# Optimization experiments

Measured on AMD Instinct MI355X. Metric: run time of the kernel, lower is better.

Reference implementation:

```python
import jax, jax.numpy as jnp
from jax import lax
import numpy as np

B, H, W, C = 32, 384, 384, 8
FIELD = 7
NUM_ITERS = 5


def setup_inputs() -> dict:
    key = jax.random.key(0)
    k1, k2, k3 = jax.random.split(key, 3)
    x = jax.random.normal(k1, (B, H, W, C), dtype=jnp.float32)
    # k_internal: [field, field, C_in, C_out]; original init is zeros, use small
    # random values so the mean-field iterations are non-trivial.
    k_internal = jax.random.normal(k2, (FIELD, FIELD, C, C), dtype=jnp.float32) * 0.02
    # 1x1 conv (k_scale) weight + bias
    k_scale_w = jax.random.normal(k3, (C, C), dtype=jnp.float32) * (1.0 / np.sqrt(C))
    k_scale_b = jnp.zeros((C,), dtype=jnp.float32)
    return {"x": x, "k_internal": k_internal, "k_scale_w": k_scale_w,
            "k_scale_b": k_scale_b, "num_iters": NUM_ITERS}


def reference(x, k_internal, k_scale_w, k_scale_b, num_iters):
    C_ = x.shape[-1]
    # off-diagonal channel-pair mask, broadcast over spatial kernel dims
    mask = (1.0 - jnp.eye(C_, dtype=x.dtype))[None, None]  # [1,1,C,C]
    k = k_internal * mask
    q = jax.nn.softmax(x, axis=-1)                 # [B,H,W,C]
    u = -jnp.log(jnp.clip(q, 1e-6, 1.0))           # unary potentials
    logits = x
    for _ in range(num_iters):
        penalty = lax.conv_general_dilated(
            q, k, window_strides=(1, 1), padding='SAME',
            dimension_numbers=('NHWC', 'HWIO', 'NHWC'))
        logits = -(u + penalty)
        logits = jnp.einsum('bhwc,cd->bhwd', logits, k_scale_w) + k_scale_b
        q = jax.nn.softmax(logits, axis=-1)
    return logits
```

## Files before the change

kernel.cpp:

```cpp
#include <hip/hip_runtime.h>
#include <math.h>

#define Cc     8
#define FIELD  7
#define PAD    3
#define TW     32
#define TH     16
#define HAW    38
#define HAH    22
#define QSTR   39
#define NSTG   (HAH*QSTR)
#define BB     32
#define HH     384
#define WW     384
#define NB     4
#define NSLOT  64
#define UCLIP  13.815510557964274f

typedef __attribute__((ext_vector_type(8))) short short8;
typedef __attribute__((ext_vector_type(4))) float f32x4;

__device__ __forceinline__ unsigned short f2bf(float f) {
    unsigned u = __float_as_uint(f);
    u += 0x7FFFu + ((u >> 16) & 1u);
    return (unsigned short)(u >> 16);
}
__device__ __forceinline__ unsigned short f2h(float f) {
    return __builtin_bit_cast(unsigned short, (_Float16)f);
}
__device__ __forceinline__ float hlo(unsigned u) {
    return (float)__builtin_bit_cast(_Float16, (unsigned short)(u & 0xFFFFu));
}
__device__ __forceinline__ float hhi(unsigned u) {
    return (float)__builtin_bit_cast(_Float16, (unsigned short)(u >> 16));
}

__global__ __launch_bounds__(256)
void prep_w(const float* __restrict__ kw, const float* __restrict__ sw,
            unsigned short* __restrict__ wtab) {
    int it = blockIdx.x * 256 + threadIdx.x;
    if (it >= NSLOT * 8) return;
    int s = it >> 3, j = it & 7;
    int dyp = s >> 3, dx = s & 7;
#pragma unroll
    for (int n = 0; n < 16; ++n) {
        int h = n >> 3, d = n & 7;
        int dy = dyp - h;
        float a = 0.f;
        if (dy >= 0 && dy < FIELD && dx < 7) {
            int tap = dy * 7 + dx;
#pragma unroll
            for (int c = 0; c < Cc; ++c) {
                float kv = (c == j) ? 0.f : kw[(tap * Cc + j) * Cc + c];
                a = fmaf(kv, sw[c * Cc + d], a);
            }
        }
        wtab[(s * 16 + n) * 8 + j] = f2bf(a);
    }
}

__global__ __launch_bounds__(256)
void init_qv(const float* __restrict__ x, const float* __restrict__ sw,
             const float* __restrict__ sb,
             uint4* __restrict__ q0, float* __restrict__ vf,
             uint4* __restrict__ vh, int half) {
    const long long HALF = (long long)BB * HH * WW / 2;
    const long long p0 = (long long)blockIdx.x * 256 + threadIdx.x;
    const long long p1 = p0 + HALF;

    const float4* xp0 = (const float4*)(x + p0 * Cc);
    const float4* xp1 = (const float4*)(x + p1 * Cc);
    float4 a0 = xp0[0], a1 = xp0[1];
    float4 b0 = xp1[0], b1 = xp1[1];

    float xa[Cc] = {a0.x, a0.y, a0.z, a0.w, a1.x, a1.y, a1.z, a1.w};
    float xb[Cc] = {b0.x, b0.y, b0.z, b0.w, b1.x, b1.y, b1.z, b1.w};

    float ma = xa[0], mb = xb[0];
#pragma unroll
    for (int c = 1; c < Cc; ++c) { ma = fmaxf(ma, xa[c]); mb = fmaxf(mb, xb[c]); }
    float sa = 0.f, sb_ = 0.f, ea[Cc], eb[Cc];
#pragma unroll
    for (int c = 0; c < Cc; ++c) {
        ea[c] = __expf(xa[c] - ma); sa += ea[c];
        eb[c] = __expf(xb[c] - mb); sb_ += eb[c];
    }
    float ia = 1.f / sa, ib = 1.f / sb_;
    uint4 qa, qb;
    qa.x = f2bf(ea[0] * ia) | ((unsigned)f2bf(ea[1] * ia) << 16);
    qa.y = f2bf(ea[2] * ia) | ((unsigned)f2bf(ea[3] * ia) << 16);
    qa.z = f2bf(ea[4] * ia) | ((unsigned)f2bf(ea[5] * ia) << 16);
    qa.w = f2bf(ea[6] * ia) | ((unsigned)f2bf(ea[7] * ia) << 16);
    qb.x = f2bf(eb[0] * ib) | ((unsigned)f2bf(eb[1] * ib) << 16);
    qb.y = f2bf(eb[2] * ib) | ((unsigned)f2bf(eb[3] * ib) << 16);
    qb.z = f2bf(eb[4] * ib) | ((unsigned)f2bf(eb[5] * ib) << 16);
    qb.w = f2bf(eb[6] * ib) | ((unsigned)f2bf(eb[7] * ib) << 16);
    q0[p0] = qa;
    q0[p1] = qb;

    float lsea = ma + __logf(sa), lseb = mb + __logf(sb_);
    float ua[Cc], ub[Cc];
#pragma unroll
    for (int c = 0; c < Cc; ++c) {
        ua[c] = fminf(lsea - xa[c], UCLIP);
        ub[c] = fminf(lseb - xb[c], UCLIP);
    }
    float va[Cc], vb[Cc];
#pragma unroll
    for (int d = 0; d < Cc; ++d) {
        float aa = sb[d], ab = sb[d];
#pragma unroll
        for (int c = 0; c < Cc; ++c) {
            float w = sw[c * Cc + d];
            aa = fmaf(-ua[c], w, aa);
            ab = fmaf(-ub[c], w, ab);
        }
        va[d] = aa; vb[d] = ab;
    }
    if (half) {
        uint4 voa, vob;
        voa.x = f2h(va[0]) | ((unsigned)f2h(va[1]) << 16);
        voa.y = f2h(va[2]) | ((unsigned)f2h(va[3]) << 16);
        voa.z = f2h(va[4]) | ((unsigned)f2h(va[5]) << 16);
        voa.w = f2h(va[6]) | ((unsigned)f2h(va[7]) << 16);
        vob.x = f2h(vb[0]) | ((unsigned)f2h(vb[1]) << 16);
        vob.y = f2h(vb[2]) | ((unsigned)f2h(vb[3]) << 16);
        vob.z = f2h(vb[4]) | ((unsigned)f2h(vb[5]) << 16);
        vob.w = f2h(vb[6]) | ((unsigned)f2h(vb[7]) << 16);
        vh[p0] = voa;
        vh[p1] = vob;
    } else {
        float4* vpa = (float4*)(vf + p0 * Cc);
        vpa[0] = make_float4(va[0], va[1], va[2], va[3]);
        vpa[1] = make_float4(va[4], va[5], va[6], va[7]);
        float4* vpb = (float4*)(vf + p1 * Cc);
        vpb[0] = make_float4(vb[0], vb[1], vb[2], vb[3]);
        vpb[1] = make_float4(vb[4], vb[5], vb[6], vb[7]);
    }
}

template<int VHALF>
__global__ __launch_bounds__(512)
void mrf_iter(const uint4* __restrict__ qin,
              const unsigned short* __restrict__ wtab,
              const void* __restrict__ vsrc,
              uint4* __restrict__ qout,
              float* __restrict__ lout,
              int last) {
    __shared__ __align__(16) uint4 qs[2][NSTG];

    const int tid = threadIdx.x;
    const int wv  = tid >> 6;
    const int l   = tid & 63;
    const int m   = l & 15;
    const int g   = l >> 4;

    const int w0 = blockIdx.x * TW;
    const int h0 = blockIdx.y * TH;
    const int b0 = blockIdx.z * NB;

    const int r0 = 4 * (wv >> 1);
    const int cx = 16 * (wv & 1);

    const int p   = g & 1;
    const int row = r0 + 2 * p + (g >> 1);
    const int px  = cx + m;
    const long long pixoff = (long long)(h0 + row) * WW + (w0 + px);
    const long long BSTR   = (long long)HH * WW;

    short8 bw[8][2];
#pragma unroll
    for (int dyq = 0; dyq < 8; ++dyq)
#pragma unroll
        for (int dxb = 0; dxb < 2; ++dxb) {
            int s = dyq * 8 + 4 * dxb + g;
            uint4 t = *(const uint4*)(wtab + (s * 16 + m) * 8);
            bw[dyq][dxb] = __builtin_bit_cast(short8, t);
        }

    const int sy0 = tid / QSTR, sx0 = tid - sy0 * QSTR;
    const int gh0 = h0 + sy0 - PAD, gw0 = w0 + sx0 - PAD;
    const bool in0 = (gh0 >= 0 && gh0 < HH && gw0 >= 0 && gw0 < WW);
    const long long off0 = (long long)gh0 * WW + gw0;
    const int  s1  = tid + 512;
    const bool has1 = (s1 < NSTG);
    const int sy1 = s1 / QSTR, sx1 = s1 - sy1 * QSTR;
    const int gh1 = h0 + sy1 - PAD, gw1 = w0 + sx1 - PAD;
    const bool in1 = has1 && (gh1 >= 0 && gh1 < HH && gw1 >= 0 && gw1 < WW);
    const long long off1 = (long long)gh1 * WW + gw1;

    const uint4* qb = qin + b0 * BSTR;
    const uint4  zz = make_uint4(0, 0, 0, 0);

    uint4 c0 = in0 ? qb[off0] : zz;
    uint4 c1 = in1 ? qb[off1] : zz;
    uint4  vhv = zz;
    float4 v0, v1;
    if constexpr (VHALF) {
        vhv = ((const uint4*)vsrc)[b0 * BSTR + pixoff];
    } else {
        const float4* vp0 = (const float4*)((const float*)vsrc + (b0 * BSTR + pixoff) * Cc);
        v0 = vp0[0]; v1 = vp0[1];
    }
    qs[0][tid] = c0;
    if (has1) qs[0][s1] = c1;
    __syncthreads();

#pragma unroll
    for (int t = 0; t < NB; ++t) {
        uint4 n0 = zz, n1 = zz, vhn = zz;
        float4 vn0 = make_float4(0.f, 0.f, 0.f, 0.f), vn1 = vn0;
        if (t + 1 < NB) {
            const uint4* qbn = qb + (t + 1) * BSTR;
            n0 = in0 ? qbn[off0] : zz;
            n1 = in1 ? qbn[off1] : zz;
            if constexpr (VHALF) {
                vhn = ((const uint4*)vsrc)[(b0 + t + 1) * BSTR + pixoff];
            } else {
                const float4* vpn = (const float4*)((const float*)vsrc + ((b0 + t + 1) * BSTR + pixoff) * Cc);
                vn0 = vpn[0]; vn1 = vpn[1];
            }
        }

        f32x4 acc0 = (f32x4){0.f, 0.f, 0.f, 0.f};
        f32x4 acc1 = (f32x4){0.f, 0.f, 0.f, 0.f};
        const uint4* Q = qs[t & 1];
        const int colbase = cx + m + g;
#pragma unroll
        for (int dyp = 0; dyp < 10; ++dyp) {
            const int rb = (r0 + dyp) * QSTR + colbase;
#pragma unroll
            for (int dxb = 0; dxb < 2; ++dxb) {
                short8 qv = *(const short8*)&Q[rb + 4 * dxb];
                if (dyp < 8)
                    acc0 = __builtin_amdgcn_mfma_f32_16x16x32_bf16(bw[dyp][dxb], qv, acc0, 0, 0, 0);
                if (dyp >= 2)
                    acc1 = __builtin_amdgcn_mfma_f32_16x16x32_bf16(bw[dyp - 2][dxb], qv, acc1, 0, 0, 0);
            }
        }

        float o[Cc];
#pragma unroll
        for (int tt = 0; tt < 4; ++tt) {
            float s0v = __shfl_xor(acc0[tt], 16);
            float s1v = __shfl_xor(acc1[tt], 16);
            o[tt]     = p ? s1v      : acc0[tt];
            o[4 + tt] = p ? acc1[tt] : s0v;
        }

        float vv[Cc];
        if constexpr (VHALF) {
            vv[0] = hlo(vhv.x); vv[1] = hhi(vhv.x);
            vv[2] = hlo(vhv.y); vv[3] = hhi(vhv.y);
            vv[4] = hlo(vhv.z); vv[5] = hhi(vhv.z);
            vv[6] = hlo(vhv.w); vv[7] = hhi(vhv.w);
        } else {
            vv[0] = v0.x; vv[1] = v0.y; vv[2] = v0.z; vv[3] = v0.w;
            vv[4] = v1.x; vv[5] = v1.y; vv[6] = v1.z; vv[7] = v1.w;
        }
#pragma unroll
        for (int d = 0; d < Cc; ++d) o[d] = vv[d] - o[d];
        const long long pix = (b0 + t) * BSTR + pixoff;
        if (last) {
            float4* op = (float4*)(lout + pix * Cc);
            op[0] = make_float4(o[0], o[1], o[2], o[3]);
            op[1] = make_float4(o[4], o[5], o[6], o[7]);
        } else {
            float mm = o[0];
#pragma unroll
            for (int d = 1; d < Cc; ++d) mm = fmaxf(mm, o[d]);
            float ss = 0.f, e[Cc];
#pragma unroll
            for (int d = 0; d < Cc; ++d) { e[d] = __expf(o[d] - mm); ss += e[d]; }
            float inv = 1.f / ss;
            uint4 qo;
            qo.x = f2bf(e[0] * inv) | ((unsigned)f2bf(e[1] * inv) << 16);
            qo.y = f2bf(e[2] * inv) | ((unsigned)f2bf(e[3] * inv) << 16);
            qo.z = f2bf(e[4] * inv) | ((unsigned)f2bf(e[5] * inv) << 16);
            qo.w = f2bf(e[6] * inv) | ((unsigned)f2bf(e[7] * inv) << 16);
            qout[pix] = qo;
        }

        if (t + 1 < NB) {
            qs[(t + 1) & 1][tid] = n0;
            if (has1) qs[(t + 1) & 1][s1] = n1;
            __syncthreads();
            if constexpr (VHALF) { vhv = vhn; } else { v0 = vn0; v1 = vn1; }
        }
    }
}

extern "C" void kernel_launch(void* const* d_in, const int* in_sizes, int n_in,
                              void* d_out, int out_size, void* d_ws, size_t ws_size,
                              hipStream_t stream) {
    (void)in_sizes; (void)n_in; (void)out_size;
    const float* x  = (const float*)d_in[0];
    const float* kw = (const float*)d_in[1];
    const float* sw = (const float*)d_in[2];
    const float* sb = (const float*)d_in[3];

    const size_t QSZ = (size_t)BB * HH * WW * 16;
    const size_t VSZ = (size_t)BB * HH * WW * 16;
    uint4* qA = (uint4*)d_ws;
    uint4* qB = (uint4*)((char*)d_ws + QSZ);

    const long long npix = (long long)BB * HH * WW;
    dim3 grid(WW / TW, HH / TH, BB / NB);

    if (ws_size >= 2 * QSZ + VSZ + 16384) {
        uint4* vh = (uint4*)((char*)d_ws + 2 * QSZ);
        unsigned short* wt = (unsigned short*)((char*)d_ws + 2 * QSZ + VSZ);
        prep_w<<<2, 256, 0, stream>>>(kw, sw, wt);
        init_qv<<<(int)(npix / 512), 256, 0, stream>>>(x, sw, sb, qA, nullptr, vh, 1);
        mrf_iter<1><<<grid, 512, 0, stream>>>(qA, wt, vh, qB, nullptr, 0);
        mrf_iter<1><<<grid, 512, 0, stream>>>(qB, wt, vh, qA, nullptr, 0);
        mrf_iter<1><<<grid, 512, 0, stream>>>(qA, wt, vh, qB, nullptr, 0);
        mrf_iter<1><<<grid, 512, 0, stream>>>(qB, wt, vh, qA, nullptr, 0);
        mrf_iter<1><<<grid, 512, 0, stream>>>(qA, wt, vh, nullptr, (float*)d_out, 1);
    } else {
        float* vbuf = (float*)d_out;
        unsigned short* wt = (unsigned short*)((char*)d_ws + 2 * QSZ);
        prep_w<<<2, 256, 0, stream>>>(kw, sw, wt);
        init_qv<<<(int)(npix / 512), 256, 0, stream>>>(x, sw, sb, qA, vbuf, nullptr, 0);
        mrf_iter<0><<<grid, 512, 0, stream>>>(qA, wt, vbuf, qB, nullptr, 0);
        mrf_iter<0><<<grid, 512, 0, stream>>>(qB, wt, vbuf, qA, nullptr, 0);
        mrf_iter<0><<<grid, 512, 0, stream>>>(qA, wt, vbuf, qB, nullptr, 0);
        mrf_iter<0><<<grid, 512, 0, stream>>>(qB, wt, vbuf, qA, nullptr, 0);
        mrf_iter<0><<<grid, 512, 0, stream>>>(qA, wt, vbuf, nullptr, (float*)d_out, 1);
    }
}
```

Baseline: 361.5 us.

## Fuse pairs of mean-field iterations into one kernel with halo recompute

```diff
diff --git a/kernel.cpp b/kernel.cpp
--- a/kernel.cpp
+++ b/kernel.cpp
@@ -6,10 +6,11 @@
 #define PAD    3
 #define TW     32
 #define TH     16
-#define HAW    38
-#define HAH    22
 #define QSTR   39
-#define NSTG   (HAH*QSTR)
+#define NSTG   (22*QSTR)
+#define Q1S    56
+#define NST1   (30*Q1S)
+#define Q2S    49
 #define BB     32
 #define HH     384
 #define WW     384
@@ -33,6 +34,21 @@
 }
 __device__ __forceinline__ float hhi(unsigned u) {
     return (float)__builtin_bit_cast(_Float16, (unsigned short)(u >> 16));
+}
+__device__ __forceinline__ uint4 softmax_pack(const float o[Cc]) {
+    float mm = o[0];
+#pragma unroll
+    for (int d = 1; d < Cc; ++d) mm = fmaxf(mm, o[d]);
+    float ss = 0.f, e[Cc];
+#pragma unroll
+    for (int d = 0; d < Cc; ++d) { e[d] = __expf(o[d] - mm); ss += e[d]; }
+    float inv = 1.f / ss;
+    uint4 qo;
+    qo.x = f2bf(e[0] * inv) | ((unsigned)f2bf(e[1] * inv) << 16);
+    qo.y = f2bf(e[2] * inv) | ((unsigned)f2bf(e[3] * inv) << 16);
+    qo.z = f2bf(e[4] * inv) | ((unsigned)f2bf(e[5] * inv) << 16);
+    qo.w = f2bf(e[6] * inv) | ((unsigned)f2bf(e[7] * inv) << 16);
+    return qo;
 }
 
 __global__ __launch_bounds__(256)
@@ -139,6 +155,127 @@
     }
 }
 
+__global__ __launch_bounds__(512)
+void mrf_pair(const uint4* __restrict__ qin,
+              const unsigned short* __restrict__ wtab,
+              const uint4* __restrict__ vh,
+              uint4* __restrict__ qout) {
+    __shared__ __align__(16) uint4 qs1[NST1];
+    __shared__ __align__(16) uint4 qs2[24 * Q2S];
+
+    const int tid = threadIdx.x;
+    const int wv  = tid >> 6;
+    const int l   = tid & 63;
+    const int m   = l & 15;
+    const int g   = l >> 4;
+    const int p   = g & 1;
+    const int hb  = g >> 1;
+
+    const int w0 = blockIdx.x * TW;
+    const int h0 = blockIdx.y * TH;
+    const int b  = blockIdx.z;
+    const long long BSTR = (long long)HH * WW;
+    const uint4 zz = make_uint4(0, 0, 0, 0);
+
+    short8 bw[8][2];
+#pragma unroll
+    for (int dyq = 0; dyq < 8; ++dyq)
+#pragma unroll
+        for (int dxb = 0; dxb < 2; ++dxb) {
+            int s = dyq * 8 + 4 * dxb + g;
+            uint4 t = *(const uint4*)(wtab + (s * 16 + m) * 8);
+            bw[dyq][dxb] = __builtin_bit_cast(short8, t);
+        }
+
+    const uint4* qb = qin + (long long)b * BSTR;
+    for (int s = tid; s < NST1; s += 512) {
+        int sy = s / Q1S, sx = s - sy * Q1S;
+        int gh = h0 + sy - 7, gw = w0 + sx - 11;
+        uint4 val = zz;
+        if (gh >= 0 && gh < HH && gw >= 0 && gw < WW)
+            val = qb[(long long)gh * WW + gw];
+        qs1[s] = val;
+    }
+    __syncthreads();
+
+    for (int u = wv; u < 18; u += 8) {
+        int rg = u / 3, cg = u - 3 * rg;
+        f32x4 acc0 = (f32x4){0.f, 0.f, 0.f, 0.f};
+        f32x4 acc1 = (f32x4){0.f, 0.f, 0.f, 0.f};
+        const int colb = 16 * cg + m + g;
+#pragma unroll
+        for (int dyp = 0; dyp < 10; ++dyp) {
+            const int rb = (4 * rg + dyp) * Q1S + colb;
+#pragma unroll
+            for (int dxb = 0; dxb < 2; ++dxb) {
+                short8 qv = *(const short8*)&qs1[rb + 4 * dxb];
+                if (dyp < 8)
+                    acc0 = __builtin_amdgcn_mfma_f32_16x16x32_bf16(bw[dyp][dxb], qv, acc0, 0, 0, 0);
+                if (dyp >= 2)
+                    acc1 = __builtin_amdgcn_mfma_f32_16x16x32_bf16(bw[dyp - 2][dxb], qv, acc1, 0, 0, 0);
+            }
+        }
+        float o[Cc];
+#pragma unroll
+        for (int tt = 0; tt < 4; ++tt) {
+            float s0v = __shfl_xor(acc0[tt], 16);
+            float s1v = __shfl_xor(acc1[tt], 16);
+            o[tt]     = p ? s1v      : acc0[tt];
+            o[4 + tt] = p ? acc1[tt] : s0v;
+        }
+        const int my = 4 * rg + 2 * p + hb;
+        const int mx = 16 * cg + m;
+        const int gy = h0 + my - 4, gx = w0 + mx - 8;
+        uint4 qo = zz;
+        if (gy >= 0 && gy < HH && gx >= 0 && gx < WW) {
+            uint4 vhv = vh[(long long)b * BSTR + (long long)gy * WW + gx];
+            o[0] = hlo(vhv.x) - o[0]; o[1] = hhi(vhv.x) - o[1];
+            o[2] = hlo(vhv.y) - o[2]; o[3] = hhi(vhv.y) - o[3];
+            o[4] = hlo(vhv.z) - o[4]; o[5] = hhi(vhv.z) - o[5];
+            o[6] = hlo(vhv.w) - o[6]; o[7] = hhi(vhv.w) - o[7];
+            qo = softmax_pack(o);
+        }
+        qs2[my * Q2S + mx] = qo;
+    }
+    __syncthreads();
+
+    const int r0 = 4 * (wv >> 1);
+    const int cx = 16 * (wv & 1);
+    const int row = r0 + 2 * p + hb;
+    const int px  = cx + m;
+    const long long pix = (long long)b * BSTR + (long long)(h0 + row) * WW + (w0 + px);
+
+    f32x4 acc0 = (f32x4){0.f, 0.f, 0.f, 0.f};
+    f32x4 acc1 = (f32x4){0.f, 0.f, 0.f, 0.f};
+    const int colb2 = cx + m + g + 5;
+#pragma unroll
+    for (int dyp = 0; dyp < 10; ++dyp) {
+        const int rb = (r0 + 1 + dyp) * Q2S + colb2;
+#pragma unroll
+        for (int dxb = 0; dxb < 2; ++dxb) {
+            short8 qv = *(const short8*)&qs2[rb + 4 * dxb];
+            if (dyp < 8)
+                acc0 = __builtin_amdgcn_mfma_f32_16x16x32_bf16(bw[dyp][dxb], qv, acc0, 0, 0, 0);
+            if (dyp >= 2)
+                acc1 = __builtin_amdgcn_mfma_f32_16x16x32_bf16(bw[dyp - 2][dxb], qv, acc1, 0, 0, 0);
+        }
+    }
+    float o[Cc];
+#pragma unroll
+    for (int tt = 0; tt < 4; ++tt) {
+        float s0v = __shfl_xor(acc0[tt], 16);
+        float s1v = __shfl_xor(acc1[tt], 16);
+        o[tt]     = p ? s1v      : acc0[tt];
+        o[4 + tt] = p ? acc1[tt] : s0v;
+    }
+    uint4 vhv = vh[pix];
+    o[0] = hlo(vhv.x) - o[0]; o[1] = hhi(vhv.x) - o[1];
+    o[2] = hlo(vhv.y) - o[2]; o[3] = hhi(vhv.y) - o[3];
+    o[4] = hlo(vhv.z) - o[4]; o[5] = hhi(vhv.z) - o[5];
+    o[6] = hlo(vhv.w) - o[6]; o[7] = hhi(vhv.w) - o[7];
+    qout[pix] = softmax_pack(o);
+}
+
 template<int VHALF>
 __global__ __launch_bounds__(512)
 void mrf_iter(const uint4* __restrict__ qin,
@@ -266,19 +403,7 @@
             op[0] = make_float4(o[0], o[1], o[2], o[3]);
             op[1] = make_float4(o[4], o[5], o[6], o[7]);
         } else {
-            float mm = o[0];
-#pragma unroll
-            for (int d = 1; d < Cc; ++d) mm = fmaxf(mm, o[d]);
-            float ss = 0.f, e[Cc];
-#pragma unroll
-            for (int d = 0; d < Cc; ++d) { e[d] = __expf(o[d] - mm); ss += e[d]; }
-            float inv = 1.f / ss;
-            uint4 qo;
-            qo.x = f2bf(e[0] * inv) | ((unsigned)f2bf(e[1] * inv) << 16);
-            qo.y = f2bf(e[2] * inv) | ((unsigned)f2bf(e[3] * inv) << 16);
-            qo.z = f2bf(e[4] * inv) | ((unsigned)f2bf(e[5] * inv) << 16);
-            qo.w = f2bf(e[6] * inv) | ((unsigned)f2bf(e[7] * inv) << 16);
-            qout[pix] = qo;
+            qout[pix] = softmax_pack(o);
         }
 
         if (t + 1 < NB) {
@@ -312,10 +437,9 @@
         unsigned short* wt = (unsigned short*)((char*)d_ws + 2 * QSZ + VSZ);
         prep_w<<<2, 256, 0, stream>>>(kw, sw, wt);
         init_qv<<<(int)(npix / 512), 256, 0, stream>>>(x, sw, sb, qA, nullptr, vh, 1);
-        mrf_iter<1><<<grid, 512, 0, stream>>>(qA, wt, vh, qB, nullptr, 0);
-        mrf_iter<1><<<grid, 512, 0, stream>>>(qB, wt, vh, qA, nullptr, 0);
-        mrf_iter<1><<<grid, 512, 0, stream>>>(qA, wt, vh, qB, nullptr, 0);
-        mrf_iter<1><<<grid, 512, 0, stream>>>(qB, wt, vh, qA, nullptr, 0);
+        dim3 gridP(WW / TW, HH / TH, BB);
+        mrf_pair<<<gridP, 512, 0, stream>>>(qA, wt, vh, qB);
+        mrf_pair<<<gridP, 512, 0, stream>>>(qB, wt, vh, qA);
         mrf_iter<1><<<grid, 512, 0, stream>>>(qA, wt, vh, nullptr, (float*)d_out, 1);
     } else {
         float* vbuf = (float*)d_out;
```

Measured after the change: 441.6 us. +22.1%, slower.
